# Performance work log

Hardware: AMD Instinct MI355X
Metric: run time of the kernel (lower is better)

The kernel has to match this reference:

```python
import jax, jax.numpy as jnp
import numpy as np

H, DI, N, R, B, L, K = 1024, 2048, 16, 64, 1, 2048, 4


def setup_inputs() -> dict:
    key = jax.random.key(0)
    ks = jax.random.split(key, 12)
    s = 0.02
    x = jax.random.normal(ks[0], (B, L, H), dtype=jnp.float32)
    in_proj_w = jax.random.normal(ks[1], (2 * DI, H), dtype=jnp.float32) * s
    in_proj_b = jax.random.normal(ks[2], (2 * DI,), dtype=jnp.float32) * s
    conv_w = jax.random.normal(ks[3], (DI, 1, K), dtype=jnp.float32) * s
    conv_b = jax.random.normal(ks[4], (DI,), dtype=jnp.float32) * s
    x_proj_w = jax.random.normal(ks[5], (R + 2 * N, DI), dtype=jnp.float32) * s
    dt_init_std = R ** (-0.5)
    dt_proj_w = jax.random.uniform(ks[6], (DI, R), dtype=jnp.float32, minval=-dt_init_std, maxval=dt_init_std)
    dt = jnp.exp(jax.random.uniform(ks[7], (DI,), dtype=jnp.float32) * (np.log(0.1) - np.log(0.001)) + np.log(0.001))
    dt = jnp.clip(dt, 0.0001, None)
    dt_proj_b = dt + jnp.log(-jnp.expm1(-dt))
    A_log = jnp.log(jnp.broadcast_to(jnp.arange(1, N + 1, dtype=jnp.float32)[None, :], (DI, N)))
    D = jnp.ones((DI,), dtype=jnp.float32)
    out_proj_w = jax.random.normal(ks[8], (H, DI), dtype=jnp.float32) * s
    return {"x": x, "in_proj_w": in_proj_w, "in_proj_b": in_proj_b, "conv_w": conv_w,
            "conv_b": conv_b, "x_proj_w": x_proj_w, "dt_proj_w": dt_proj_w,
            "dt_proj_b": dt_proj_b, "A_log": A_log, "D": D, "out_proj_w": out_proj_w}


def _mamba_fwd(x, in_proj_w, in_proj_b, conv_w, conv_b, x_proj_w, dt_proj_w, dt_proj_b, A_log, D, out_proj_w):
    b, l, _ = x.shape
    x_and_res = x @ in_proj_w.T + in_proj_b               # [b, l, 2*DI]
    xc, res = jnp.split(x_and_res, 2, axis=-1)
    # causal depthwise conv1d (padding K-1 then truncate to l == left-pad only)
    xt = jnp.transpose(xc, (0, 2, 1))                     # [b, DI, l]
    conv = jax.lax.conv_general_dilated(
        xt, conv_w, window_strides=(1,), padding=[(K - 1, 0)],
        dimension_numbers=("NCH", "OIH", "NCH"), feature_group_count=DI)
    conv = conv + conv_b[None, :, None]
    xs = jnp.transpose(jax.nn.silu(conv), (0, 2, 1))      # [b, l, DI]
    # SSM
    A = -jnp.exp(A_log.astype(jnp.float32))               # [DI, N]
    x_dbl = xs @ x_proj_w.T                               # [b, l, R+2N]
    delta, Bm, Cm = jnp.split(x_dbl, [R, R + N], axis=-1)
    delta = jax.nn.softplus(delta @ dt_proj_w.T + dt_proj_b)   # [b, l, DI]
    deltaA = jnp.exp(delta[..., None] * A[None, None])         # [b, l, DI, N]
    deltaB_u = delta[..., None] * Bm[:, :, None, :] * xs[..., None]

    def comb(c1, c2):
        a1, u1 = c1
        a2, u2 = c2
        return a2 * a1, a2 * u1 + u2

    _, h = jax.lax.associative_scan(comb, (deltaA, deltaB_u), axis=1)
    y = jnp.einsum("bldn,bln->bld", h, Cm) + xs * D.astype(jnp.float32)
    y = y * jax.nn.silu(res)
    return y @ out_proj_w.T                               # [b, l, H]


def reference(x, in_proj_w, in_proj_b, conv_w, conv_b, x_proj_w, dt_proj_w, dt_proj_b, A_log, D, out_proj_w):
    return _mamba_fwd(x, in_proj_w, in_proj_b, conv_w, conv_b, x_proj_w,
                      dt_proj_w, dt_proj_b, A_log, D, out_proj_w)
```

## Files before the change

kernel.cpp:

```cpp
#include <hip/hip_runtime.h>
#include <hip/hip_bf16.h>
#include <math.h>

#define H_DIM 1024
#define DI    2048
#define NS    16
#define RR    64
#define LL    2048
#define NC    32
#define CL    64
#define KSPL  16

typedef __bf16 bf16x8 __attribute__((ext_vector_type(8)));
typedef __bf16 bf16x4 __attribute__((ext_vector_type(4)));
typedef float  f32x4  __attribute__((ext_vector_type(4)));

__device__ __forceinline__ float silu_f(float x)  { return x / (1.f + __expf(-x)); }
__device__ __forceinline__ float softplus_f(float x) {
    const float l = __logf(1.f + __expf(x));
    return x > 15.f ? x : l;
}

__device__ __forceinline__ void gload16(const void* g, void* l) {
    __builtin_amdgcn_global_load_lds(
        (const __attribute__((address_space(1))) void*)g,
        (__attribute__((address_space(3))) void*)l, 16, 0, 0);
}

__device__ __forceinline__ void f2b4(const float* __restrict__ in,
                                     __bf16* __restrict__ out)
{
    float4 v = *(const float4*)in;
    bf16x4 o;
    o[0] = (__bf16)v.x; o[1] = (__bf16)v.y; o[2] = (__bf16)v.z; o[3] = (__bf16)v.w;
    *(bf16x4*)out = o;
}

#define SEG0 (LL * H_DIM)
#define SEG1 (2 * DI * H_DIM)
#define SEG2 (H_DIM * DI)
#define SEG3 (DI * RR)
#define SEG4 (128 * DI)
#define CUM0 SEG0
#define CUM1 (CUM0 + SEG1)
#define CUM2 (CUM1 + SEG2)
#define CUM3 (CUM2 + SEG3)
#define CUMT (CUM3 + SEG4)

__global__ __launch_bounds__(256) void convert_all_k(
    const float* __restrict__ x,    const float* __restrict__ in_w,
    const float* __restrict__ outw, const float* __restrict__ dtw,
    const float* __restrict__ xpw,
    __bf16* __restrict__ x_bf,    __bf16* __restrict__ inw_bf,
    __bf16* __restrict__ outw_bf, __bf16* __restrict__ dtw_bf,
    __bf16* __restrict__ xpw_pad)
{
    const int i = (blockIdx.x * 256 + threadIdx.x) * 4;
    if (i < CUM0) {
        f2b4(x + i, x_bf + i);
    } else if (i < CUM1) {
        const int o = i - CUM0;  f2b4(in_w + o, inw_bf + o);
    } else if (i < CUM2) {
        const int o = i - CUM1;  f2b4(outw + o, outw_bf + o);
    } else if (i < CUM3) {
        const int o = i - CUM2;  f2b4(dtw + o, dtw_bf + o);
    } else if (i < CUMT) {
        const int o = i - CUM3;
        const int row = o >> 11;
        if (row < 96) {
            f2b4(xpw + o, xpw_pad + o);
        } else {
            bf16x4 z; z[0] = z[1] = z[2] = z[3] = (__bf16)0.f;
            *(bf16x4*)&xpw_pad[o] = z;
        }
    }
}

__global__ __launch_bounds__(256) void reduce_xdbl_k(
    const float* __restrict__ part, float* __restrict__ xdbl,
    __bf16* __restrict__ xdbl_bf)
{
    const int idx = blockIdx.x * 256 + threadIdx.x;
    float s = 0.f;
    #pragma unroll
    for (int z = 0; z < KSPL; ++z) s += part[(size_t)z * (LL * 96) + idx];
    xdbl[idx] = s;
    xdbl_bf[idx] = (__bf16)s;
}

template<int BIAS, int ACT>
__global__ __launch_bounds__(256) void gemm_bf16_nt(
    const __bf16* __restrict__ A, int lda,
    const __bf16* __restrict__ W, int ldw,
    const float* __restrict__ bias,
    float* __restrict__ C, int ldc,
    int K)
{
    __shared__ __bf16 smA[128 * 32];
    __shared__ __bf16 smB[128 * 32];
    const int t    = threadIdx.x;
    const int lane = t & 63;
    const int m0 = blockIdx.y * 128, n0 = blockIdx.x * 128;
    const int wr = ((t >> 6) >> 1) * 64;
    const int wc = ((t >> 6) & 1) * 64;

    const int srow = t >> 2;
    const int skof = (t & 3) * 8;
    const int lds_base = (t >> 6) * 512;

    const int offA = (wr + (lane & 15)) * 32 + ((lane >> 4) * 8);
    const int offB = (wc + (lane & 15)) * 32 + ((lane >> 4) * 8);

    f32x4 acc[4][4] = {};

    for (int k0 = 0; k0 < K; k0 += 32) {
        gload16(A + (size_t)(m0 + srow)      * lda + k0 + skof, &smA[lds_base]);
        gload16(A + (size_t)(m0 + 64 + srow) * lda + k0 + skof, &smA[2048 + lds_base]);
        gload16(W + (size_t)(n0 + srow)      * ldw + k0 + skof, &smB[lds_base]);
        gload16(W + (size_t)(n0 + 64 + srow) * ldw + k0 + skof, &smB[2048 + lds_base]);
        __syncthreads();

        bf16x8 af[4], bfr[4];
        #pragma unroll
        for (int m = 0; m < 4; ++m) af[m]  = *(const bf16x8*)&smA[offA + m * 512];
        #pragma unroll
        for (int n = 0; n < 4; ++n) bfr[n] = *(const bf16x8*)&smB[offB + n * 512];
        #pragma unroll
        for (int m = 0; m < 4; ++m)
            #pragma unroll
            for (int n = 0; n < 4; ++n)
                acc[m][n] = __builtin_amdgcn_mfma_f32_16x16x32_bf16(
                    af[m], bfr[n], acc[m][n], 0, 0, 0);
        __syncthreads();
    }

    const int rbase = m0 + wr + ((lane >> 4) << 2);
    const int cbase = n0 + wc + (lane & 15);
    #pragma unroll
    for (int n = 0; n < 4; ++n) {
        const int col = cbase + n * 16;
        const float bv = BIAS ? bias[col] : 0.f;
        #pragma unroll
        for (int m = 0; m < 4; ++m) {
            #pragma unroll
            for (int j = 0; j < 4; ++j) {
                float v = acc[m][n][j] + bv;
                if (ACT == 1) v = softplus_f(v);
                C[(size_t)(rbase + m * 16 + j) * ldc + col] = v;
            }
        }
    }
}

template<int BIAS, int ACT, int SPLITK>
__global__ __launch_bounds__(256) void gemm64_bf16_nt(
    const __bf16* __restrict__ A, int lda,
    const __bf16* __restrict__ W, int ldw,
    const float* __restrict__ bias,
    float* __restrict__ C, int ldc, int ncols, size_t pstride,
    int K)
{
    __shared__ __bf16 smA[64 * 32];
    __shared__ __bf16 smB[128 * 32];
    const int t    = threadIdx.x;
    const int lane = t & 63;
    const int m0 = blockIdx.y * 64, n0 = blockIdx.x * 128;
    const int wr = ((t >> 6) >> 1) * 32;
    const int wc = ((t >> 6) & 1) * 64;

    const int srow = t >> 2;
    const int skof = (t & 3) * 8;
    const int lds_base = (t >> 6) * 512;

    const int offA = (wr + (lane & 15)) * 32 + ((lane >> 4) * 8);
    const int offB = (wc + (lane & 15)) * 32 + ((lane >> 4) * 8);

    const int kseg  = K / SPLITK;
    const int kbase = (SPLITK > 1) ? blockIdx.z * kseg : 0;

    f32x4 acc[2][4] = {};

    for (int k0 = kbase; k0 < kbase + kseg; k0 += 32) {
        gload16(A + (size_t)(m0 + srow)      * lda + k0 + skof, &smA[lds_base]);
        gload16(W + (size_t)(n0 + srow)      * ldw + k0 + skof, &smB[lds_base]);
        gload16(W + (size_t)(n0 + 64 + srow) * ldw + k0 + skof, &smB[2048 + lds_base]);
        __syncthreads();

        bf16x8 af[2], bfr[4];
        #pragma unroll
        for (int m = 0; m < 2; ++m) af[m]  = *(const bf16x8*)&smA[offA + m * 512];
        #pragma unroll
        for (int n = 0; n < 4; ++n) bfr[n] = *(const bf16x8*)&smB[offB + n * 512];
        #pragma unroll
        for (int m = 0; m < 2; ++m)
            #pragma unroll
            for (int n = 0; n < 4; ++n)
                acc[m][n] = __builtin_amdgcn_mfma_f32_16x16x32_bf16(
                    af[m], bfr[n], acc[m][n], 0, 0, 0);
        __syncthreads();
    }

    float* Cp = C + ((SPLITK > 1) ? (size_t)blockIdx.z * pstride : 0);
    const int rbase = m0 + wr + ((lane >> 4) << 2);
    const int cbase = n0 + wc + (lane & 15);
    #pragma unroll
    for (int n = 0; n < 4; ++n) {
        const int col = cbase + n * 16;
        if (col >= ncols) continue;
        const float bv = BIAS ? bias[col] : 0.f;
        #pragma unroll
        for (int m = 0; m < 2; ++m) {
            #pragma unroll
            for (int j = 0; j < 4; ++j) {
                float v = acc[m][n][j] + bv;
                if (ACT == 1) v = softplus_f(v);
                Cp[(size_t)(rbase + m * 16 + j) * ldc + col] = v;
            }
        }
    }
}

__global__ __launch_bounds__(256) void conv_silu_k(
    const float* __restrict__ xr, const float* __restrict__ cw,
    const float* __restrict__ cb, float* __restrict__ xs,
    __bf16* __restrict__ xs_bf)
{
    const int idx = blockIdx.x * 256 + threadIdx.x;
    const int l = idx >> 11;
    const int d = idx & (DI - 1);
    float acc = cb[d];
    const float w0 = cw[d*4+0], w1 = cw[d*4+1], w2 = cw[d*4+2], w3 = cw[d*4+3];
    if (l >= 3) acc = fmaf(xr[(size_t)(l-3)*(2*DI) + d], w0, acc);
    if (l >= 2) acc = fmaf(xr[(size_t)(l-2)*(2*DI) + d], w1, acc);
    if (l >= 1) acc = fmaf(xr[(size_t)(l-1)*(2*DI) + d], w2, acc);
    acc = fmaf(xr[(size_t)l*(2*DI) + d], w3, acc);
    const float s = silu_f(acc);
    xs[idx] = s;
    xs_bf[idx] = (__bf16)s;
}

__global__ __launch_bounds__(256) void scan1_k(
    const float* __restrict__ delta, const float* __restrict__ xs,
    const float* __restrict__ A_log, const float* __restrict__ xdbl,
    float* __restrict__ P, float* __restrict__ S)
{
    const int d = blockIdx.x * 256 + threadIdx.x;
    const int c = blockIdx.y;
    float A[NS];
    #pragma unroll
    for (int n = 0; n < NS; ++n) A[n] = -__expf(A_log[d * NS + n]);
    float h[NS] = {};
    float ap[NS];
    #pragma unroll
    for (int n = 0; n < NS; ++n) ap[n] = 1.f;

    const int l0 = c * CL;
    for (int l = l0; l < l0 + CL; ++l) {
        const float dt = delta[(size_t)l * DI + d];
        const float u  = xs[(size_t)l * DI + d];
        const float du = dt * u;
        #pragma unroll
        for (int n = 0; n < NS; ++n) {
            const float Bn = xdbl[(size_t)l * 96 + RR + n];
            const float dA = __expf(dt * A[n]);
            h[n]  = fmaf(dA, h[n], du * Bn);
            ap[n] *= dA;
        }
    }
    const size_t base = ((size_t)c * DI + d) * NS;
    #pragma unroll
    for (int n = 0; n < NS; ++n) { P[base + n] = ap[n]; S[base + n] = h[n]; }
}

__global__ __launch_bounds__(256) void scan2_k(
    const float* __restrict__ P, const float* __restrict__ S, float* __restrict__ Hp)
{
    const int idx = blockIdx.x * 256 + threadIdx.x;
    float h = 0.f;
    for (int c = 0; c < NC; ++c) {
        const size_t o = (size_t)c * DI * NS + idx;
        Hp[o] = h;
        h = fmaf(P[o], h, S[o]);
    }
}

__global__ __launch_bounds__(256) void scan3_k(
    const float* __restrict__ delta, const float* __restrict__ xs,
    const float* __restrict__ A_log, const float* __restrict__ xdbl,
    const float* __restrict__ Hp, const float* __restrict__ xr,
    const float* __restrict__ Dp, __bf16* __restrict__ y_bf)
{
    const int d = blockIdx.x * 256 + threadIdx.x;
    const int c = blockIdx.y;
    float A[NS];
    #pragma unroll
    for (int n = 0; n < NS; ++n) A[n] = -__expf(A_log[d * NS + n]);
    float h[NS];
    const size_t base = ((size_t)c * DI + d) * NS;
    #pragma unroll
    for (int n = 0; n < NS; ++n) h[n] = Hp[base + n];
    const float Dd = Dp[d];

    const int l0 = c * CL;
    for (int l = l0; l < l0 + CL; ++l) {
        const float dt = delta[(size_t)l * DI + d];
        const float u  = xs[(size_t)l * DI + d];
        const float du = dt * u;
        float acc = 0.f;
        #pragma unroll
        for (int n = 0; n < NS; ++n) {
            const float Bn = xdbl[(size_t)l * 96 + RR + n];
            const float Cn = xdbl[(size_t)l * 96 + RR + NS + n];
            const float dA = __expf(dt * A[n]);
            h[n] = fmaf(dA, h[n], du * Bn);
            acc  = fmaf(h[n], Cn, acc);
        }
        float yv = fmaf(u, Dd, acc);
        const float r = xr[(size_t)l * (2*DI) + DI + d];
        yv *= silu_f(r);
        y_bf[(size_t)l * DI + d] = (__bf16)yv;
    }
}

extern "C" void kernel_launch(void* const* d_in, const int* in_sizes, int n_in,
                              void* d_out, int out_size, void* d_ws, size_t ws_size,
                              hipStream_t stream)
{
    const float* x        = (const float*)d_in[0];
    const float* in_w     = (const float*)d_in[1];
    const float* in_b     = (const float*)d_in[2];
    const float* conv_w   = (const float*)d_in[3];
    const float* conv_b   = (const float*)d_in[4];
    const float* xproj_w  = (const float*)d_in[5];
    const float* dtproj_w = (const float*)d_in[6];
    const float* dtproj_b = (const float*)d_in[7];
    const float* A_log    = (const float*)d_in[8];
    const float* Dp       = (const float*)d_in[9];
    const float* outw     = (const float*)d_in[10];
    float* out = (float*)d_out;

    float* ws    = (float*)d_ws;
    float* xr    = ws;
    float* xs    = xr    + (size_t)LL * 2 * DI;
    float* xdbl  = xs    + (size_t)LL * DI;
    float* delta = xdbl  + (size_t)LL * 96;
    float* P     = delta + (size_t)LL * DI;
    float* S     = P     + (size_t)NC * DI * NS;
    float* Hp    = S     + (size_t)NC * DI * NS;
    float* xpart = delta;
    __bf16* x_bf    = (__bf16*)(Hp + (size_t)NC * DI * NS);
    __bf16* inw_bf  = x_bf    + (size_t)LL * H_DIM;
    __bf16* outw_bf = inw_bf  + (size_t)2 * DI * H_DIM;
    __bf16* dtw_bf  = outw_bf + (size_t)H_DIM * DI;
    __bf16* xdbl_bf = dtw_bf  + (size_t)DI * RR;
    __bf16* y_bf    = xdbl_bf + (size_t)LL * 96;
    __bf16* xs_bf   = y_bf    + (size_t)LL * DI;
    __bf16* xpw_pad = xs_bf   + (size_t)LL * DI;

    const dim3 blk(256);

    convert_all_k<<<dim3(CUMT / 1024), blk, 0, stream>>>(
        x, in_w, outw, dtproj_w, xproj_w,
        x_bf, inw_bf, outw_bf, dtw_bf, xpw_pad);

    gemm_bf16_nt<1,0><<<dim3((2*DI)/128, LL/128), blk, 0, stream>>>(
        x_bf, H_DIM, inw_bf, H_DIM, in_b, xr, 2*DI, H_DIM);

    conv_silu_k<<<dim3((LL*DI)/256), blk, 0, stream>>>(xr, conv_w, conv_b, xs, xs_bf);

    gemm64_bf16_nt<0,0,KSPL><<<dim3(1, LL/64, KSPL), blk, 0, stream>>>(
        xs_bf, DI, xpw_pad, DI, nullptr, xpart, 96, 96, (size_t)LL * 96, DI);
    reduce_xdbl_k<<<dim3((LL * 96) / 256), blk, 0, stream>>>(xpart, xdbl, xdbl_bf);

    gemm64_bf16_nt<1,1,1><<<dim3(DI/128, LL/64), blk, 0, stream>>>(
        xdbl_bf, 96, dtw_bf, RR, dtproj_b, delta, DI, DI, 0, RR);

    scan1_k<<<dim3(DI/256, NC), blk, 0, stream>>>(delta, xs, A_log, xdbl, P, S);
    scan2_k<<<dim3((DI*NS)/256), blk, 0, stream>>>(P, S, Hp);
    scan3_k<<<dim3(DI/256, NC), blk, 0, stream>>>(delta, xs, A_log, xdbl, Hp, xr, Dp, y_bf);

    gemm64_bf16_nt<0,0,1><<<dim3(H_DIM/128, LL/64), blk, 0, stream>>>(
        y_bf, DI, outw_bf, DI, nullptr, out, H_DIM, H_DIM, 0, DI);
}
```

Before: 273.4 us.

## Store in-projection outputs and conv activations as bf16, vectorize conv

```diff
diff --git a/kernel.cpp b/kernel.cpp
--- a/kernel.cpp
+++ b/kernel.cpp
@@ -88,13 +88,12 @@
     xdbl_bf[idx] = (__bf16)s;
 }
 
-template<int BIAS, int ACT>
-__global__ __launch_bounds__(256) void gemm_bf16_nt(
-    const __bf16* __restrict__ A, int lda,
-    const __bf16* __restrict__ W, int ldw,
+__global__ __launch_bounds__(256) void gemm_inproj_k(
+    const __bf16* __restrict__ A,
+    const __bf16* __restrict__ W,
     const float* __restrict__ bias,
-    float* __restrict__ C, int ldc,
-    int K)
+    __bf16* __restrict__ xc_bf,
+    __bf16* __restrict__ res_bf)
 {
     __shared__ __bf16 smA[128 * 32];
     __shared__ __bf16 smB[128 * 32];
@@ -113,11 +112,11 @@
 
     f32x4 acc[4][4] = {};
 
-    for (int k0 = 0; k0 < K; k0 += 32) {
-        gload16(A + (size_t)(m0 + srow)      * lda + k0 + skof, &smA[lds_base]);
-        gload16(A + (size_t)(m0 + 64 + srow) * lda + k0 + skof, &smA[2048 + lds_base]);
-        gload16(W + (size_t)(n0 + srow)      * ldw + k0 + skof, &smB[lds_base]);
-        gload16(W + (size_t)(n0 + 64 + srow) * ldw + k0 + skof, &smB[2048 + lds_base]);
+    for (int k0 = 0; k0 < H_DIM; k0 += 32) {
+        gload16(A + (size_t)(m0 + srow)      * H_DIM + k0 + skof, &smA[lds_base]);
+        gload16(A + (size_t)(m0 + 64 + srow) * H_DIM + k0 + skof, &smA[2048 + lds_base]);
+        gload16(W + (size_t)(n0 + srow)      * H_DIM + k0 + skof, &smB[lds_base]);
+        gload16(W + (size_t)(n0 + 64 + srow) * H_DIM + k0 + skof, &smB[2048 + lds_base]);
         __syncthreads();
 
         bf16x8 af[4], bfr[4];
@@ -134,21 +133,20 @@
         __syncthreads();
     }
 
+    __bf16* outp = (n0 < DI) ? xc_bf : res_bf;
+    const int ncol0 = (n0 < DI) ? n0 : n0 - DI;
     const int rbase = m0 + wr + ((lane >> 4) << 2);
-    const int cbase = n0 + wc + (lane & 15);
+    const int cbase = ncol0 + wc + (lane & 15);
     #pragma unroll
     for (int n = 0; n < 4; ++n) {
         const int col = cbase + n * 16;
-        const float bv = BIAS ? bias[col] : 0.f;
-        #pragma unroll
-        for (int m = 0; m < 4; ++m) {
+        const float bv = bias[(n0 < DI ? 0 : DI) + col];
+        #pragma unroll
+        for (int m = 0; m < 4; ++m)
             #pragma unroll
-            for (int j = 0; j < 4; ++j) {
-                float v = acc[m][n][j] + bv;
-                if (ACT == 1) v = softplus_f(v);
-                C[(size_t)(rbase + m * 16 + j) * ldc + col] = v;
-            }
-        }
+            for (int j = 0; j < 4; ++j)
+                outp[(size_t)(rbase + m * 16 + j) * DI + col] =
+                    (__bf16)(acc[m][n][j] + bv);
     }
 }
 
@@ -221,26 +219,45 @@
 }
 
 __global__ __launch_bounds__(256) void conv_silu_k(
-    const float* __restrict__ xr, const float* __restrict__ cw,
-    const float* __restrict__ cb, float* __restrict__ xs,
-    __bf16* __restrict__ xs_bf)
+    const __bf16* __restrict__ xc, const float* __restrict__ cw,
+    const float* __restrict__ cb, __bf16* __restrict__ xs_bf)
 {
     const int idx = blockIdx.x * 256 + threadIdx.x;
-    const int l = idx >> 11;
-    const int d = idx & (DI - 1);
-    float acc = cb[d];
-    const float w0 = cw[d*4+0], w1 = cw[d*4+1], w2 = cw[d*4+2], w3 = cw[d*4+3];
-    if (l >= 3) acc = fmaf(xr[(size_t)(l-3)*(2*DI) + d], w0, acc);
-    if (l >= 2) acc = fmaf(xr[(size_t)(l-2)*(2*DI) + d], w1, acc);
-    if (l >= 1) acc = fmaf(xr[(size_t)(l-1)*(2*DI) + d], w2, acc);
-    acc = fmaf(xr[(size_t)l*(2*DI) + d], w3, acc);
-    const float s = silu_f(acc);
-    xs[idx] = s;
-    xs_bf[idx] = (__bf16)s;
+    const int l  = idx >> 8;
+    const int d0 = (idx & 255) * 8;
+
+    float r0[8] = {}, r1[8] = {}, r2[8] = {}, r3[8];
+    bf16x8 v;
+    if (l >= 3) { v = *(const bf16x8*)&xc[(size_t)(l-3)*DI + d0];
+                  #pragma unroll
+                  for (int j = 0; j < 8; ++j) r0[j] = (float)v[j]; }
+    if (l >= 2) { v = *(const bf16x8*)&xc[(size_t)(l-2)*DI + d0];
+                  #pragma unroll
+                  for (int j = 0; j < 8; ++j) r1[j] = (float)v[j]; }
+    if (l >= 1) { v = *(const bf16x8*)&xc[(size_t)(l-1)*DI + d0];
+                  #pragma unroll
+                  for (int j = 0; j < 8; ++j) r2[j] = (float)v[j]; }
+    v = *(const bf16x8*)&xc[(size_t)l*DI + d0];
+    #pragma unroll
+    for (int j = 0; j < 8; ++j) r3[j] = (float)v[j];
+
+    bf16x8 o;
+    #pragma unroll
+    for (int j = 0; j < 8; ++j) {
+        const int d = d0 + j;
+        float4 w = *(const float4*)&cw[d * 4];
+        float a = cb[d];
+        a = fmaf(r0[j], w.x, a);
+        a = fmaf(r1[j], w.y, a);
+        a = fmaf(r2[j], w.z, a);
+        a = fmaf(r3[j], w.w, a);
+        o[j] = (__bf16)silu_f(a);
+    }
+    *(bf16x8*)&xs_bf[(size_t)l*DI + d0] = o;
 }
 
 __global__ __launch_bounds__(256) void scan1_k(
-    const float* __restrict__ delta, const float* __restrict__ xs,
+    const float* __restrict__ delta, const __bf16* __restrict__ xs,
     const float* __restrict__ A_log, const float* __restrict__ xdbl,
     float* __restrict__ P, float* __restrict__ S)
 {
@@ -257,7 +274,7 @@
     const int l0 = c * CL;
     for (int l = l0; l < l0 + CL; ++l) {
         const float dt = delta[(size_t)l * DI + d];
-        const float u  = xs[(size_t)l * DI + d];
+        const float u  = (float)xs[(size_t)l * DI + d];
         const float du = dt * u;
         #pragma unroll
         for (int n = 0; n < NS; ++n) {
@@ -285,9 +302,9 @@
 }
 
 __global__ __launch_bounds__(256) void scan3_k(
-    const float* __restrict__ delta, const float* __restrict__ xs,
+    const float* __restrict__ delta, const __bf16* __restrict__ xs,
     const float* __restrict__ A_log, const float* __restrict__ xdbl,
-    const float* __restrict__ Hp, const float* __restrict__ xr,
+    const float* __restrict__ Hp, const __bf16* __restrict__ res_bf,
     const float* __restrict__ Dp, __bf16* __restrict__ y_bf)
 {
     const int d = blockIdx.x * 256 + threadIdx.x;
@@ -304,7 +321,7 @@
     const int l0 = c * CL;
     for (int l = l0; l < l0 + CL; ++l) {
         const float dt = delta[(size_t)l * DI + d];
-        const float u  = xs[(size_t)l * DI + d];
+        const float u  = (float)xs[(size_t)l * DI + d];
         const float du = dt * u;
         float acc = 0.f;
         #pragma unroll
@@ -316,7 +333,7 @@
             acc  = fmaf(h[n], Cn, acc);
         }
         float yv = fmaf(u, Dd, acc);
-        const float r = xr[(size_t)l * (2*DI) + DI + d];
+        const float r = (float)res_bf[(size_t)l * DI + d];
         yv *= silu_f(r);
         y_bf[(size_t)l * DI + d] = (__bf16)yv;
     }
@@ -340,11 +357,9 @@
     float* out = (float*)d_out;
 
     float* ws    = (float*)d_ws;
-    float* xr    = ws;
-    float* xs    = xr    + (size_t)LL * 2 * DI;
-    float* xdbl  = xs    + (size_t)LL * DI;
-    float* delta = xdbl  + (size_t)LL * 96;
-    float* P     = delta + (size_t)LL * DI;
+    float* delta = ws;
+    float* xdbl  = delta + (size_t)LL * DI;
+    float* P     = xdbl  + (size_t)LL * 96;
     float* S     = P     + (size_t)NC * DI * NS;
     float* Hp    = S     + (size_t)NC * DI * NS;
     float* xpart = delta;
@@ -355,7 +370,9 @@
     __bf16* xdbl_bf = dtw_bf  + (size_t)DI * RR;
     __bf16* y_bf    = xdbl_bf + (size_t)LL * 96;
     __bf16* xs_bf   = y_bf    + (size_t)LL * DI;
-    __bf16* xpw_pad = xs_bf   + (size_t)LL * DI;
+    __bf16* xc_bf   = xs_bf   + (size_t)LL * DI;
+    __bf16* res_bf  = xc_bf   + (size_t)LL * DI;
+    __bf16* xpw_pad = res_bf  + (size_t)LL * DI;
 
     const dim3 blk(256);
 
@@ -363,10 +380,10 @@
         x, in_w, outw, dtproj_w, xproj_w,
         x_bf, inw_bf, outw_bf, dtw_bf, xpw_pad);
 
-    gemm_bf16_nt<1,0><<<dim3((2*DI)/128, LL/128), blk, 0, stream>>>(
-        x_bf, H_DIM, inw_bf, H_DIM, in_b, xr, 2*DI, H_DIM);
-
-    conv_silu_k<<<dim3((LL*DI)/256), blk, 0, stream>>>(xr, conv_w, conv_b, xs, xs_bf);
+    gemm_inproj_k<<<dim3((2*DI)/128, LL/128), blk, 0, stream>>>(
+        x_bf, inw_bf, in_b, xc_bf, res_bf);
+
+    conv_silu_k<<<dim3((LL*DI)/(8*256)), blk, 0, stream>>>(xc_bf, conv_w, conv_b, xs_bf);
 
     gemm64_bf16_nt<0,0,KSPL><<<dim3(1, LL/64, KSPL), blk, 0, stream>>>(
         xs_bf, DI, xpw_pad, DI, nullptr, xpart, 96, 96, (size_t)LL * 96, DI);
@@ -375,9 +392,9 @@
     gemm64_bf16_nt<1,1,1><<<dim3(DI/128, LL/64), blk, 0, stream>>>(
         xdbl_bf, 96, dtw_bf, RR, dtproj_b, delta, DI, DI, 0, RR);
 
-    scan1_k<<<dim3(DI/256, NC), blk, 0, stream>>>(delta, xs, A_log, xdbl, P, S);
+    scan1_k<<<dim3(DI/256, NC), blk, 0, stream>>>(delta, xs_bf, A_log, xdbl, P, S);
     scan2_k<<<dim3((DI*NS)/256), blk, 0, stream>>>(P, S, Hp);
-    scan3_k<<<dim3(DI/256, NC), blk, 0, stream>>>(delta, xs, A_log, xdbl, Hp, xr, Dp, y_bf);
+    scan3_k<<<dim3(DI/256, NC), blk, 0, stream>>>(delta, xs_bf, A_log, xdbl, Hp, res_bf, Dp, y_bf);
 
     gemm64_bf16_nt<0,0,1><<<dim3(H_DIM/128, LL/64), blk, 0, stream>>>(
         y_bf, DI, outw_bf, DI, nullptr, out, H_DIM, H_DIM, 0, DI);
```

Result: no change. 269.0 us (-1.6%).
